# Performance work log

Hardware: AMD Instinct MI355X
Metric: run time of the kernel (lower is better)

Reference implementation:

```python
import jax, jax.numpy as jnp
import numpy as np

FEAT_STRIDE = 32  # 520 // 16
POOL = 7          # adaptive_avg_pool2d target (7,7)
C = 8             # channels consumed as (2 classes x 4 coords)


def setup_inputs() -> dict:
    key = jax.random.key(0)
    k1, k2, k3 = jax.random.split(key, 3)
    H = W = 1024
    conv_out = jax.random.normal(k1, (1, C, H, W), dtype=jnp.float32)
    n = 8192
    # sample pixel-space coords in [0, H*FEAT_STRIDE) and sort so min<=max per axis
    ys = jnp.sort(jax.random.randint(k2, (n, 2), 0, H * FEAT_STRIDE), axis=1)
    xs = jnp.sort(jax.random.randint(k3, (n, 2), 0, W * FEAT_STRIDE), axis=1)
    rois = jnp.stack([ys[:, 0], xs[:, 0], ys[:, 1], xs[:, 1]], axis=1).astype(jnp.int64)
    return {"conv_out": conv_out, "rois": rois}


def _adaptive_bounds(start, length):
    # PyTorch adaptive_avg_pool2d bin edges over [start, start+length)
    j = jnp.arange(POOL)
    lo = start + (j * length) // POOL
    hi = start + ((j + 1) * length + POOL - 1) // POOL  # ceil div
    return lo, hi


def _forward(conv_out, rois):
    r = rois // FEAT_STRIDE
    x = conv_out[0]  # [C, H, W]
    # summed-area table, padded so sat[:, y, x] = sum over [0:y, 0:x)
    sat = jnp.pad(jnp.cumsum(jnp.cumsum(x, axis=1), axis=2),
                  ((0, 0), (1, 0), (1, 0)))  # [C, H+1, W+1]

    def pool_one(roi):
        ymin, xmin = roi[0], roi[1]
        ymax, xmax = roi[2] + 1, roi[3] + 1  # exclusive ends
        ylo, yhi = _adaptive_bounds(ymin, ymax - ymin)
        xlo, xhi = _adaptive_bounds(xmin, xmax - xmin)
        # 7x7 bin sums via inclusion-exclusion on SAT -> [C,7,7]
        s = (sat[:, yhi[:, None], xhi[None, :]]
             - sat[:, ylo[:, None], xhi[None, :]]
             - sat[:, yhi[:, None], xlo[None, :]]
             + sat[:, ylo[:, None], xlo[None, :]])
        area = ((yhi - ylo)[:, None] * (xhi - xlo)[None, :]).astype(s.dtype)
        block7 = s / area                       # adaptive_avg_pool2d -> (7,7)
        return block7.mean(axis=(1, 2))         # adaptive_avg_pool2d -> (1,1), [C]

    pooled = jax.vmap(pool_one)(r)              # [n, C]
    return pooled.reshape(-1, 2, 4)


def reference(conv_out, rois):
    return _forward(conv_out, rois)
```

## Files before the change

### kernel.cpp

```cpp
#include <hip/hip_runtime.h>
#include <cstddef>
#include <cstdint>


#define SATW_PAD 1026
#define W8   8200
#define W8P  8208
#define NCH  8

#define NBAND 64
#define BROWS 16
#define CHUNK_F32 1024
#define NCHUNK 9

__global__ __launch_bounds__(256) void rowscan_kernel(const float* __restrict__ in,
                                                      float* __restrict__ sat) {
    const int y    = blockIdx.x;
    const int t    = threadIdx.x;
    const int lane = t & 63;
    const int wv   = t >> 6;

    __shared__ float lds[NCH][1024];

    for (int k = 0; k < 2; ++k) {
        const int c = wv * 2 + k;
        const float4* r4 = (const float4*)(in + ((size_t)c * 1024 + y) * 1024);
        double chunkbase = 0.0;
#pragma unroll
        for (int j = 0; j < 4; ++j) {
            float4 a = r4[lane + 64 * j];
            double v0 = a.x, v1 = a.y, v2 = a.z, v3 = a.w;
            double s = v0 + v1 + v2 + v3;
            double ps = s;
#pragma unroll
            for (int off = 1; off < 64; off <<= 1) {
                double n = __shfl_up(ps, off, 64);
                if (lane >= off) ps += n;
            }
            double base = chunkbase + ps - s;
            double p0 = base + v0, p1 = p0 + v1, p2 = p1 + v2, p3 = p2 + v3;
            ((float4*)lds[c])[lane + 64 * j] =
                make_float4((float)p0, (float)p1, (float)p2, (float)p3);
            chunkbase += __shfl(ps, 63, 64);
        }
    }
    __syncthreads();

    float* orow = sat + (size_t)(y + 1) * W8P;
    for (int f4 = t; f4 < W8P / 4; f4 += 256) {
        int f = f4 * 4;
        float4 o;
        float* po = (float*)&o;
#pragma unroll
        for (int j = 0; j < 4; ++j) {
            int ff = f + j;
            int x = ff >> 3, c = ff & 7;
            po[j] = (x >= 1 && x <= 1024) ? lds[c][x - 1] : 0.0f;
        }
        ((float4*)orow)[f4] = o;
    }
}

__global__ __launch_bounds__(256) void band_sum(const float* __restrict__ sat,
                                                double* __restrict__ bsum) {
    const int c = blockIdx.x;
    const int b = blockIdx.y;
    const int t = threadIdx.x;
    const int col0 = c * CHUNK_F32 + t * 4;
    if (col0 >= W8) return;

    const float* p = sat + (size_t)(1 + b * BROWS) * W8P + col0;
    float4 v[BROWS];
#pragma unroll
    for (int k = 0; k < BROWS; ++k)
        v[k] = *(const float4*)(p + (size_t)k * W8P);

    double s0 = 0, s1 = 0, s2 = 0, s3 = 0;
#pragma unroll
    for (int k = 0; k < BROWS; ++k) {
        s0 += v[k].x; s1 += v[k].y; s2 += v[k].z; s3 += v[k].w;
    }

    double* o = bsum + (size_t)b * W8P + col0;
    double2 lo, hi;
    lo.x = s0; lo.y = s1; hi.x = s2; hi.y = s3;
    *(double2*)o       = lo;
    *((double2*)o + 1) = hi;
}

__global__ __launch_bounds__(64) void band_prefix(double* __restrict__ bsum) {
    const int lane = threadIdx.x;
    const int rg   = lane >> 3;
    const int s    = lane & 7;
    const size_t base = (size_t)blockIdx.x * 16 + (size_t)s * 2;

    double2 v[8];
#pragma unroll
    for (int k = 0; k < 8; ++k)
        v[k] = *(const double2*)(bsum + (size_t)(rg * 8 + k) * W8P + base);

    double i0 = 0, i1 = 0;
    double incl0[8], incl1[8];
#pragma unroll
    for (int k = 0; k < 8; ++k) {
        i0 += v[k].x; i1 += v[k].y;
        incl0[k] = i0; incl1[k] = i1;
    }

    double a0 = i0, a1 = i1;
#pragma unroll
    for (int off = 8; off <= 32; off <<= 1) {
        double u0 = __shfl_up(a0, off, 64);
        double u1 = __shfl_up(a1, off, 64);
        if (lane >= off) { a0 += u0; a1 += u1; }
    }
    const double base0 = a0 - i0, base1 = a1 - i1;

#pragma unroll
    for (int k = 0; k < 8; ++k) {
        double2 e;
        e.x = base0 + incl0[k] - v[k].x;
        e.y = base1 + incl1[k] - v[k].y;
        *(double2*)(bsum + (size_t)(rg * 8 + k) * W8P + base) = e;
    }
}

__global__ __launch_bounds__(256) void band_apply(float* __restrict__ sat,
                                                  const double* __restrict__ bpre) {
    const int c = blockIdx.x;
    const int b = blockIdx.y;
    const int t = threadIdx.x;
    const int col0 = c * CHUNK_F32 + t * 4;
    if (col0 >= W8) return;

    const double* q = bpre + (size_t)b * W8P + col0;
    double2 qlo = *(const double2*)q;
    double2 qhi = *((const double2*)q + 1);
    double a0 = qlo.x, a1 = qlo.y, a2 = qhi.x, a3 = qhi.y;

    float* p = sat + (size_t)(1 + b * BROWS) * W8P + col0;
    float4 v[BROWS];
#pragma unroll
    for (int k = 0; k < BROWS; ++k)
        v[k] = *(const float4*)(p + (size_t)k * W8P);

#pragma unroll
    for (int k = 0; k < BROWS; ++k) {
        a0 += v[k].x; a1 += v[k].y; a2 += v[k].z; a3 += v[k].w;
        *(float4*)(p + (size_t)k * W8P) =
            make_float4((float)a0, (float)a1, (float)a2, (float)a3);
    }

    if (b == 0)
        *(float4*)(sat + col0) = make_float4(0.f, 0.f, 0.f, 0.f);
}

__global__ __launch_bounds__(256) void pool_kernel(const float* __restrict__ sat,
                                                   const int* __restrict__ rois,
                                                   float* __restrict__ out,
                                                   int n_roi) {
    int lane = threadIdx.x & 63;
    int roi  = (blockIdx.x * blockDim.x + threadIdx.x) >> 6;
    if (roi >= n_roi) return;

    const int4 rv = ((const int4*)rois)[roi];
    int ymin = rv.x >> 5;
    int xmin = rv.y >> 5;
    int Ly   = (rv.z >> 5) + 1 - ymin;
    int Lx   = (rv.w >> 5) + 1 - xmin;

    float acc[NCH];
#pragma unroll
    for (int c = 0; c < NCH; ++c) acc[c] = 0.0f;

    if (lane < 49) {
        int by = lane / 7;
        int bx = lane - by * 7;
        int ylo = ymin + (by * Ly) / 7;
        int yhi = ymin + ((by + 1) * Ly + 6) / 7;
        int xlo = xmin + (bx * Lx) / 7;
        int xhi = xmin + ((bx + 1) * Lx + 6) / 7;
        float inv = 1.0f / (float)((yhi - ylo) * (xhi - xlo));

        float4 a[2], b[2], c4[2], d[2];
        const float4* hh = (const float4*)(sat + ((size_t)yhi * SATW_PAD + xhi) * NCH);
        const float4* lh = (const float4*)(sat + ((size_t)ylo * SATW_PAD + xhi) * NCH);
        const float4* hl = (const float4*)(sat + ((size_t)yhi * SATW_PAD + xlo) * NCH);
        const float4* ll = (const float4*)(sat + ((size_t)ylo * SATW_PAD + xlo) * NCH);
        a[0] = hh[0]; a[1] = hh[1];
        b[0] = lh[0]; b[1] = lh[1];
        c4[0] = hl[0]; c4[1] = hl[1];
        d[0] = ll[0]; d[1] = ll[1];
        const float* fa = (const float*)a;
        const float* fb = (const float*)b;
        const float* fc = (const float*)c4;
        const float* fd = (const float*)d;
#pragma unroll
        for (int c = 0; c < NCH; ++c)
            acc[c] = (fa[c] - fb[c] - fc[c] + fd[c]) * inv;
    }

#pragma unroll
    for (int off = 32; off; off >>= 1) {
#pragma unroll
        for (int c = 0; c < NCH; ++c) acc[c] += __shfl_down(acc[c], off, 64);
    }

    if (lane == 0) {
        const float k = 1.0f / 49.0f;
        float4* po = (float4*)(out + (size_t)roi * NCH);
        po[0] = make_float4(acc[0] * k, acc[1] * k, acc[2] * k, acc[3] * k);
        po[1] = make_float4(acc[4] * k, acc[5] * k, acc[6] * k, acc[7] * k);
    }
}

extern "C" void kernel_launch(void* const* d_in, const int* in_sizes, int n_in,
                              void* d_out, int out_size, void* d_ws, size_t ws_size,
                              hipStream_t stream) {
    const float* conv = (const float*)d_in[0];
    const int*   rois = (const int*)d_in[1];
    float*       out  = (float*)d_out;
    int n_roi = in_sizes[1] / 4;

    float*  sat  = (float*)d_ws;
    double* bsum = (double*)((char*)d_ws + 33652992);

    rowscan_kernel<<<1024, 256, 0, stream>>>(conv, sat);
    band_sum   <<<dim3(NCHUNK, NBAND), 256, 0, stream>>>(sat, bsum);
    band_prefix<<<513, 64, 0, stream>>>(bsum);
    band_apply <<<dim3(NCHUNK, NBAND), 256, 0, stream>>>(sat, bsum);
    pool_kernel<<<(n_roi + 3) / 4, 256, 0, stream>>>(sat, rois, out, n_roi);
}
```

Measured before the change: 117.0 us.

## Fuse SAT build and ROI pooling into one cooperative kernel with grid syncs

Replaces the five separate launches (row scan, band sum, band prefix, band apply, pool) with a single persistent cooperative kernel. Grid-wide syncs separate the phases, and each phase uses grid-stride loops. The aim is to remove launch gaps and inter-kernel drain/fill overhead. In exchange, every phase is limited to the occupancy-derived grid size (up to 4 blocks per CU across 256 CUs), and the kernel pays the cost of four grid barriers; the old multi-kernel path is kept as a fallback.

```diff
diff --git a/kernel.cpp b/kernel.cpp
--- a/kernel.cpp
+++ b/kernel.cpp
@@ -1,6 +1,9 @@
 #include <hip/hip_runtime.h>
+#include <hip/hip_cooperative_groups.h>
 #include <cstddef>
 #include <cstdint>
+
+namespace cg = cooperative_groups;
 
 
 #define SATW_PAD 1026
@@ -12,6 +15,197 @@
 #define BROWS 16
 #define CHUNK_F32 1024
 #define NCHUNK 9
+#define NUNIT (NCHUNK * NBAND)
+
+__global__ __launch_bounds__(256, 2)
+void fused_sat_pool(const float* __restrict__ in, const int* __restrict__ rois,
+                    float* __restrict__ out, float* __restrict__ sat,
+                    double* __restrict__ bsum, int n_roi) {
+    cg::grid_group grid = cg::this_grid();
+    const int G    = gridDim.x;
+    const int g    = blockIdx.x;
+    const int t    = threadIdx.x;
+    const int lane = t & 63;
+    const int wv   = t >> 6;
+
+    __shared__ float lds[NCH][1024];
+
+    for (int y = g; y < 1024; y += G) {
+        for (int k = 0; k < 2; ++k) {
+            const int c = wv * 2 + k;
+            const float4* r4 = (const float4*)(in + ((size_t)c * 1024 + y) * 1024);
+            double chunkbase = 0.0;
+#pragma unroll
+            for (int j = 0; j < 4; ++j) {
+                float4 a = r4[lane + 64 * j];
+                double v0 = a.x, v1 = a.y, v2 = a.z, v3 = a.w;
+                double s = v0 + v1 + v2 + v3;
+                double ps = s;
+#pragma unroll
+                for (int off = 1; off < 64; off <<= 1) {
+                    double n = __shfl_up(ps, off, 64);
+                    if (lane >= off) ps += n;
+                }
+                double base = chunkbase + ps - s;
+                double p0 = base + v0, p1 = p0 + v1, p2 = p1 + v2, p3 = p2 + v3;
+                ((float4*)lds[c])[lane + 64 * j] =
+                    make_float4((float)p0, (float)p1, (float)p2, (float)p3);
+                chunkbase += __shfl(ps, 63, 64);
+            }
+        }
+        __syncthreads();
+
+        float* orow = sat + (size_t)(y + 1) * W8P;
+        for (int f4 = t; f4 < W8P / 4; f4 += 256) {
+            int f = f4 * 4;
+            float4 o;
+            float* po = (float*)&o;
+#pragma unroll
+            for (int j = 0; j < 4; ++j) {
+                int ff = f + j;
+                int x = ff >> 3, c = ff & 7;
+                po[j] = (x >= 1 && x <= 1024) ? lds[c][x - 1] : 0.0f;
+            }
+            ((float4*)orow)[f4] = o;
+        }
+        __syncthreads();
+    }
+    grid.sync();
+
+    for (int u = g; u < NUNIT; u += G) {
+        const int c = u >> 6, b = u & 63;
+        const int col0 = c * CHUNK_F32 + t * 4;
+        if (col0 < W8) {
+            const float* p = sat + (size_t)(1 + b * BROWS) * W8P + col0;
+            double s0 = 0, s1 = 0, s2 = 0, s3 = 0;
+#pragma unroll
+            for (int k = 0; k < BROWS; ++k) {
+                float4 v = *(const float4*)(p + (size_t)k * W8P);
+                s0 += v.x; s1 += v.y; s2 += v.z; s3 += v.w;
+            }
+            double* o = bsum + (size_t)b * W8P + col0;
+            double2 lo, hi;
+            lo.x = s0; lo.y = s1; hi.x = s2; hi.y = s3;
+            *(double2*)o       = lo;
+            *((double2*)o + 1) = hi;
+        }
+    }
+    grid.sync();
+
+    for (int lc = g * 4 + wv; lc < 513; lc += G * 4) {
+        const int rg = lane >> 3;
+        const int s  = lane & 7;
+        const size_t base = (size_t)lc * 16 + (size_t)s * 2;
+
+        double2 v[8];
+#pragma unroll
+        for (int k = 0; k < 8; ++k)
+            v[k] = *(const double2*)(bsum + (size_t)(rg * 8 + k) * W8P + base);
+
+        double i0 = 0, i1 = 0;
+        double incl0[8], incl1[8];
+#pragma unroll
+        for (int k = 0; k < 8; ++k) {
+            i0 += v[k].x; i1 += v[k].y;
+            incl0[k] = i0; incl1[k] = i1;
+        }
+        double a0 = i0, a1 = i1;
+#pragma unroll
+        for (int off = 8; off <= 32; off <<= 1) {
+            double u0 = __shfl_up(a0, off, 64);
+            double u1 = __shfl_up(a1, off, 64);
+            if (lane >= off) { a0 += u0; a1 += u1; }
+        }
+        const double b0 = a0 - i0, b1 = a1 - i1;
+#pragma unroll
+        for (int k = 0; k < 8; ++k) {
+            double2 e;
+            e.x = b0 + incl0[k] - v[k].x;
+            e.y = b1 + incl1[k] - v[k].y;
+            *(double2*)(bsum + (size_t)(rg * 8 + k) * W8P + base) = e;
+        }
+    }
+    grid.sync();
+
+    for (int u = g; u < NUNIT; u += G) {
+        const int c = u >> 6, b = u & 63;
+        const int col0 = c * CHUNK_F32 + t * 4;
+        if (col0 < W8) {
+            const double* q = bsum + (size_t)b * W8P + col0;
+            double2 qlo = *(const double2*)q;
+            double2 qhi = *((const double2*)q + 1);
+            double a0 = qlo.x, a1 = qlo.y, a2 = qhi.x, a3 = qhi.y;
+
+            float* p = sat + (size_t)(1 + b * BROWS) * W8P + col0;
+            float4 v[BROWS];
+#pragma unroll
+            for (int k = 0; k < BROWS; ++k)
+                v[k] = *(const float4*)(p + (size_t)k * W8P);
+#pragma unroll
+            for (int k = 0; k < BROWS; ++k) {
+                a0 += v[k].x; a1 += v[k].y; a2 += v[k].z; a3 += v[k].w;
+                *(float4*)(p + (size_t)k * W8P) =
+                    make_float4((float)a0, (float)a1, (float)a2, (float)a3);
+            }
+            if (b == 0)
+                *(float4*)(sat + col0) = make_float4(0.f, 0.f, 0.f, 0.f);
+        }
+    }
+    grid.sync();
+
+    for (int u = g; u < (n_roi + 3) / 4; u += G) {
+        const int roi = u * 4 + wv;
+        if (roi < n_roi) {
+            const int4 rv = ((const int4*)rois)[roi];
+            int ymin = rv.x >> 5;
+            int xmin = rv.y >> 5;
+            int Ly   = (rv.z >> 5) + 1 - ymin;
+            int Lx   = (rv.w >> 5) + 1 - xmin;
+
+            float acc[NCH];
+#pragma unroll
+            for (int c = 0; c < NCH; ++c) acc[c] = 0.0f;
+
+            if (lane < 49) {
+                int by = lane / 7;
+                int bx = lane - by * 7;
+                int ylo = ymin + (by * Ly) / 7;
+                int yhi = ymin + ((by + 1) * Ly + 6) / 7;
+                int xlo = xmin + (bx * Lx) / 7;
+                int xhi = xmin + ((bx + 1) * Lx + 6) / 7;
+                float inv = 1.0f / (float)((yhi - ylo) * (xhi - xlo));
+
+                float4 a[2], b[2], c4[2], d[2];
+                const float4* hh = (const float4*)(sat + ((size_t)yhi * SATW_PAD + xhi) * NCH);
+                const float4* lh = (const float4*)(sat + ((size_t)ylo * SATW_PAD + xhi) * NCH);
+                const float4* hl = (const float4*)(sat + ((size_t)yhi * SATW_PAD + xlo) * NCH);
+                const float4* ll = (const float4*)(sat + ((size_t)ylo * SATW_PAD + xlo) * NCH);
+                a[0] = hh[0]; a[1] = hh[1];
+                b[0] = lh[0]; b[1] = lh[1];
+                c4[0] = hl[0]; c4[1] = hl[1];
+                d[0] = ll[0]; d[1] = ll[1];
+                const float* fa = (const float*)a;
+                const float* fb = (const float*)b;
+                const float* fc = (const float*)c4;
+                const float* fd = (const float*)d;
+#pragma unroll
+                for (int c = 0; c < NCH; ++c)
+                    acc[c] = (fa[c] - fb[c] - fc[c] + fd[c]) * inv;
+            }
+#pragma unroll
+            for (int off = 32; off; off >>= 1) {
+#pragma unroll
+                for (int c = 0; c < NCH; ++c) acc[c] += __shfl_down(acc[c], off, 64);
+            }
+            if (lane == 0) {
+                const float k = 1.0f / 49.0f;
+                float4* po = (float4*)(out + (size_t)roi * NCH);
+                po[0] = make_float4(acc[0] * k, acc[1] * k, acc[2] * k, acc[3] * k);
+                po[1] = make_float4(acc[4] * k, acc[5] * k, acc[6] * k, acc[7] * k);
+            }
+        }
+    }
+}
 
 __global__ __launch_bounds__(256) void rowscan_kernel(const float* __restrict__ in,
                                                       float* __restrict__ sat) {
@@ -19,9 +213,7 @@
     const int t    = threadIdx.x;
     const int lane = t & 63;
     const int wv   = t >> 6;
-
     __shared__ float lds[NCH][1024];
-
     for (int k = 0; k < 2; ++k) {
         const int c = wv * 2 + k;
         const float4* r4 = (const float4*)(in + ((size_t)c * 1024 + y) * 1024);
@@ -45,7 +237,6 @@
         }
     }
     __syncthreads();
-
     float* orow = sat + (size_t)(y + 1) * W8P;
     for (int f4 = t; f4 < W8P / 4; f4 += 256) {
         int f = f4 * 4;
@@ -63,96 +254,65 @@
 
 __global__ __launch_bounds__(256) void band_sum(const float* __restrict__ sat,
                                                 double* __restrict__ bsum) {
-    const int c = blockIdx.x;
-    const int b = blockIdx.y;
-    const int t = threadIdx.x;
+    const int c = blockIdx.x, b = blockIdx.y, t = threadIdx.x;
     const int col0 = c * CHUNK_F32 + t * 4;
     if (col0 >= W8) return;
-
     const float* p = sat + (size_t)(1 + b * BROWS) * W8P + col0;
-    float4 v[BROWS];
-#pragma unroll
-    for (int k = 0; k < BROWS; ++k)
-        v[k] = *(const float4*)(p + (size_t)k * W8P);
-
     double s0 = 0, s1 = 0, s2 = 0, s3 = 0;
 #pragma unroll
     for (int k = 0; k < BROWS; ++k) {
-        s0 += v[k].x; s1 += v[k].y; s2 += v[k].z; s3 += v[k].w;
-    }
-
+        float4 v = *(const float4*)(p + (size_t)k * W8P);
+        s0 += v.x; s1 += v.y; s2 += v.z; s3 += v.w;
+    }
     double* o = bsum + (size_t)b * W8P + col0;
-    double2 lo, hi;
-    lo.x = s0; lo.y = s1; hi.x = s2; hi.y = s3;
-    *(double2*)o       = lo;
-    *((double2*)o + 1) = hi;
+    double2 lo, hi; lo.x = s0; lo.y = s1; hi.x = s2; hi.y = s3;
+    *(double2*)o = lo; *((double2*)o + 1) = hi;
 }
 
 __global__ __launch_bounds__(64) void band_prefix(double* __restrict__ bsum) {
     const int lane = threadIdx.x;
-    const int rg   = lane >> 3;
-    const int s    = lane & 7;
+    const int rg = lane >> 3, s = lane & 7;
     const size_t base = (size_t)blockIdx.x * 16 + (size_t)s * 2;
-
     double2 v[8];
 #pragma unroll
     for (int k = 0; k < 8; ++k)
         v[k] = *(const double2*)(bsum + (size_t)(rg * 8 + k) * W8P + base);
-
-    double i0 = 0, i1 = 0;
-    double incl0[8], incl1[8];
+    double i0 = 0, i1 = 0; double incl0[8], incl1[8];
+#pragma unroll
+    for (int k = 0; k < 8; ++k) { i0 += v[k].x; i1 += v[k].y; incl0[k] = i0; incl1[k] = i1; }
+    double a0 = i0, a1 = i1;
+#pragma unroll
+    for (int off = 8; off <= 32; off <<= 1) {
+        double u0 = __shfl_up(a0, off, 64), u1 = __shfl_up(a1, off, 64);
+        if (lane >= off) { a0 += u0; a1 += u1; }
+    }
+    const double b0 = a0 - i0, b1 = a1 - i1;
 #pragma unroll
     for (int k = 0; k < 8; ++k) {
-        i0 += v[k].x; i1 += v[k].y;
-        incl0[k] = i0; incl1[k] = i1;
-    }
-
-    double a0 = i0, a1 = i1;
-#pragma unroll
-    for (int off = 8; off <= 32; off <<= 1) {
-        double u0 = __shfl_up(a0, off, 64);
-        double u1 = __shfl_up(a1, off, 64);
-        if (lane >= off) { a0 += u0; a1 += u1; }
-    }
-    const double base0 = a0 - i0, base1 = a1 - i1;
-
-#pragma unroll
-    for (int k = 0; k < 8; ++k) {
-        double2 e;
-        e.x = base0 + incl0[k] - v[k].x;
-        e.y = base1 + incl1[k] - v[k].y;
+        double2 e; e.x = b0 + incl0[k] - v[k].x; e.y = b1 + incl1[k] - v[k].y;
         *(double2*)(bsum + (size_t)(rg * 8 + k) * W8P + base) = e;
     }
 }
 
 __global__ __launch_bounds__(256) void band_apply(float* __restrict__ sat,
                                                   const double* __restrict__ bpre) {
-    const int c = blockIdx.x;
-    const int b = blockIdx.y;
-    const int t = threadIdx.x;
+    const int c = blockIdx.x, b = blockIdx.y, t = threadIdx.x;
     const int col0 = c * CHUNK_F32 + t * 4;
     if (col0 >= W8) return;
-
     const double* q = bpre + (size_t)b * W8P + col0;
-    double2 qlo = *(const double2*)q;
-    double2 qhi = *((const double2*)q + 1);
+    double2 qlo = *(const double2*)q; double2 qhi = *((const double2*)q + 1);
     double a0 = qlo.x, a1 = qlo.y, a2 = qhi.x, a3 = qhi.y;
-
     float* p = sat + (size_t)(1 + b * BROWS) * W8P + col0;
     float4 v[BROWS];
 #pragma unroll
-    for (int k = 0; k < BROWS; ++k)
-        v[k] = *(const float4*)(p + (size_t)k * W8P);
-
+    for (int k = 0; k < BROWS; ++k) v[k] = *(const float4*)(p + (size_t)k * W8P);
 #pragma unroll
     for (int k = 0; k < BROWS; ++k) {
         a0 += v[k].x; a1 += v[k].y; a2 += v[k].z; a3 += v[k].w;
         *(float4*)(p + (size_t)k * W8P) =
             make_float4((float)a0, (float)a1, (float)a2, (float)a3);
     }
-
-    if (b == 0)
-        *(float4*)(sat + col0) = make_float4(0.f, 0.f, 0.f, 0.f);
+    if (b == 0) *(float4*)(sat + col0) = make_float4(0.f, 0.f, 0.f, 0.f);
 }
 
 __global__ __launch_bounds__(256) void pool_kernel(const float* __restrict__ sat,
@@ -162,50 +322,35 @@
     int lane = threadIdx.x & 63;
     int roi  = (blockIdx.x * blockDim.x + threadIdx.x) >> 6;
     if (roi >= n_roi) return;
-
     const int4 rv = ((const int4*)rois)[roi];
-    int ymin = rv.x >> 5;
-    int xmin = rv.y >> 5;
-    int Ly   = (rv.z >> 5) + 1 - ymin;
-    int Lx   = (rv.w >> 5) + 1 - xmin;
-
+    int ymin = rv.x >> 5, xmin = rv.y >> 5;
+    int Ly = (rv.z >> 5) + 1 - ymin, Lx = (rv.w >> 5) + 1 - xmin;
     float acc[NCH];
 #pragma unroll
     for (int c = 0; c < NCH; ++c) acc[c] = 0.0f;
-
     if (lane < 49) {
-        int by = lane / 7;
-        int bx = lane - by * 7;
-        int ylo = ymin + (by * Ly) / 7;
-        int yhi = ymin + ((by + 1) * Ly + 6) / 7;
-        int xlo = xmin + (bx * Lx) / 7;
-        int xhi = xmin + ((bx + 1) * Lx + 6) / 7;
+        int by = lane / 7, bx = lane - by * 7;
+        int ylo = ymin + (by * Ly) / 7, yhi = ymin + ((by + 1) * Ly + 6) / 7;
+        int xlo = xmin + (bx * Lx) / 7, xhi = xmin + ((bx + 1) * Lx + 6) / 7;
         float inv = 1.0f / (float)((yhi - ylo) * (xhi - xlo));
-
         float4 a[2], b[2], c4[2], d[2];
         const float4* hh = (const float4*)(sat + ((size_t)yhi * SATW_PAD + xhi) * NCH);
         const float4* lh = (const float4*)(sat + ((size_t)ylo * SATW_PAD + xhi) * NCH);
         const float4* hl = (const float4*)(sat + ((size_t)yhi * SATW_PAD + xlo) * NCH);
         const float4* ll = (const float4*)(sat + ((size_t)ylo * SATW_PAD + xlo) * NCH);
-        a[0] = hh[0]; a[1] = hh[1];
-        b[0] = lh[0]; b[1] = lh[1];
-        c4[0] = hl[0]; c4[1] = hl[1];
-        d[0] = ll[0]; d[1] = ll[1];
-        const float* fa = (const float*)a;
-        const float* fb = (const float*)b;
-        const float* fc = (const float*)c4;
-        const float* fd = (const float*)d;
+        a[0] = hh[0]; a[1] = hh[1]; b[0] = lh[0]; b[1] = lh[1];
+        c4[0] = hl[0]; c4[1] = hl[1]; d[0] = ll[0]; d[1] = ll[1];
+        const float* fa = (const float*)a; const float* fb = (const float*)b;
+        const float* fc = (const float*)c4; const float* fd = (const float*)d;
 #pragma unroll
         for (int c = 0; c < NCH; ++c)
             acc[c] = (fa[c] - fb[c] - fc[c] + fd[c]) * inv;
     }
-
 #pragma unroll
     for (int off = 32; off; off >>= 1) {
 #pragma unroll
         for (int c = 0; c < NCH; ++c) acc[c] += __shfl_down(acc[c], off, 64);
     }
-
     if (lane == 0) {
         const float k = 1.0f / 49.0f;
         float4* po = (float4*)(out + (size_t)roi * NCH);
@@ -225,9 +370,35 @@
     float*  sat  = (float*)d_ws;
     double* bsum = (double*)((char*)d_ws + 33652992);
 
-    rowscan_kernel<<<1024, 256, 0, stream>>>(conv, sat);
-    band_sum   <<<dim3(NCHUNK, NBAND), 256, 0, stream>>>(sat, bsum);
-    band_prefix<<<513, 64, 0, stream>>>(bsum);
-    band_apply <<<dim3(NCHUNK, NBAND), 256, 0, stream>>>(sat, bsum);
-    pool_kernel<<<(n_roi + 3) / 4, 256, 0, stream>>>(sat, rois, out, n_roi);
-}
+    static int coop_grid = -1;
+    if (coop_grid == -1) {
+        int nb = 0;
+        hipError_t e = hipOccupancyMaxActiveBlocksPerMultiprocessor(
+            &nb, fused_sat_pool, 256, 0);
+        if (e == hipSuccess && nb >= 1) {
+            if (nb > 4) nb = 4;
+            coop_grid = nb * 256;
+        } else {
+            coop_grid = 0;
+        }
+    }
+
+    bool done = false;
+    if (coop_grid > 0) {
+        void* args[] = {(void*)&conv, (void*)&rois, (void*)&out,
+                        (void*)&sat,  (void*)&bsum, (void*)&n_roi};
+        hipError_t e = hipLaunchCooperativeKernel(
+            (const void*)fused_sat_pool, dim3(coop_grid), dim3(256),
+            args, 0, stream);
+        if (e == hipSuccess) done = true;
+        else coop_grid = 0;
+    }
+
+    if (!done) {
+        rowscan_kernel<<<1024, 256, 0, stream>>>(conv, sat);
+        band_sum   <<<dim3(NCHUNK, NBAND), 256, 0, stream>>>(sat, bsum);
+        band_prefix<<<513, 64, 0, stream>>>(bsum);
+        band_apply <<<dim3(NCHUNK, NBAND), 256, 0, stream>>>(sat, bsum);
+        pool_kernel<<<(n_roi + 3) / 4, 256, 0, stream>>>(sat, rois, out, n_roi);
+    }
+}
```

New measurement: 371.2 us. +217.2%, slower.
